# Kernel tuning notes

Measured on AMD Instinct MI355X. Metric: run time of the kernel, lower is better.

## Reference

```python
import jax, jax.numpy as jnp
import numpy as np

NEG = -9e15


def setup_inputs() -> dict:
    key = jax.random.key(0)
    k1, k2, k3, k4, k5 = jax.random.split(key, 5)
    N, D_IN, D_OUT = 8192, 512, 128
    x = jax.random.normal(k1, (N, D_IN), dtype=jnp.float32)
    adj = jax.random.randint(k2, (N, N), 0, 2, dtype=jnp.int32)
    W_fc = jax.random.normal(k3, (D_IN, D_OUT), dtype=jnp.float32) * (1.0 / np.sqrt(D_IN))
    w_a1 = jax.random.normal(k4, (D_OUT,), dtype=jnp.float32) * (1.0 / np.sqrt(D_OUT))
    w_a2 = jax.random.normal(k5, (D_OUT,), dtype=jnp.float32) * (1.0 / np.sqrt(D_OUT))
    return {"x": x, "adj": adj, "W_fc": W_fc, "w_a1": w_a1, "w_a2": w_a2}


def reference(x, adj, W_fc, w_a1, w_a2):
    # h = fc(x): [N, d_out]
    h = x @ W_fc
    # a1, a2: [N] projections; outer-sum scores a1[i] + a2[j] -> [N, N]
    a1 = h @ w_a1
    a2 = h @ w_a2
    scores = a1[:, None] + a2[None, :]
    # adjacency mask + row softmax
    scores = jnp.where(adj > 0, scores, jnp.float32(NEG))
    attention = jax.nn.softmax(scores, axis=-1)
    # weighted aggregation: [N, N] @ [N, d_out]
    out = attention @ h
    return out  # act == 'None', so no relu
```

## Files before the change

kernel.cpp:

```cpp
#include <hip/hip_runtime.h>
#include <hip/hip_bf16.h>


#define NN 8192
#define DIN 512
#define DOUT 128

typedef __attribute__((ext_vector_type(4))) int   int4v;
typedef __attribute__((ext_vector_type(4))) float f32x4;
typedef __attribute__((ext_vector_type(8))) short bf16x8;

static __device__ __forceinline__ unsigned short f2bf(float f) {
    unsigned u = __float_as_uint(f);
    return (unsigned short)((u + 0x7FFFu + ((u >> 16) & 1u)) >> 16);
}
static __device__ __forceinline__ float bf2f(unsigned short b) {
    return __uint_as_float((unsigned)b << 16);
}
static __device__ __forceinline__ void gload_lds16(const void* g, void* l) {
    __builtin_amdgcn_global_load_lds(
        (const __attribute__((address_space(1))) unsigned*)g,
        (__attribute__((address_space(3))) unsigned*)l, 16, 0, 0);
}
static __device__ __forceinline__ int4v ntld(const int* p) {
    return __builtin_nontemporal_load(reinterpret_cast<const int4v*>(p));
}
static __device__ __forceinline__ f32x4 ntldf4(const float* p) {
    return __builtin_nontemporal_load(reinterpret_cast<const f32x4*>(p));
}

__global__ __launch_bounds__(256) void k_cvtW(const float* __restrict__ W,
                                              unsigned short* __restrict__ WT) {
    __shared__ float s[8][128];
    const int t  = threadIdx.x;
    const int k0 = blockIdx.x * 8;
    {
        int idx = t * 4;
        int k = idx >> 7, d = idx & 127;
        float4 v = *reinterpret_cast<const float4*>(&W[(size_t)(k0 + k) * DOUT + d]);
        *reinterpret_cast<float4*>(&s[k][d]) = v;
    }
    __syncthreads();
    const int d  = t & 127;
    const int pl = t >> 7;
    unsigned short o[8];
    #pragma unroll
    for (int kk = 0; kk < 8; ++kk) {
        float f = s[kk][d];
        unsigned short hb = f2bf(f);
        o[kk] = pl ? f2bf(f - bf2f(hb)) : hb;
    }
    *reinterpret_cast<uint4*>(&WT[(size_t)pl * 128 * DIN + (size_t)d * DIN + k0]) =
        *reinterpret_cast<const uint4*>(o);
}

__global__ __launch_bounds__(256) void k_h(const float* __restrict__ x,
                                           const unsigned short* __restrict__ WT,
                                           const float* __restrict__ wa2,
                                           unsigned short* __restrict__ Gt) {
    __shared__ __align__(16) char xs[32768];
    __shared__ float red[4][16];
    __shared__ float es[16];
    const int t = threadIdx.x;
    const int w = t >> 6, l = t & 63;
    const int c = l & 15, g = l >> 4;
    const int j0 = blockIdx.x * 16;

    f32x4 xv[8];
    #pragma unroll
    for (int s = 0; s < 8; ++s) {
        int ii = t + s * 256;
        int r = ii >> 7, k4 = ii & 127;
        xv[s] = ntldf4(&x[(size_t)(j0 + r) * DIN + k4 * 4]);
    }
    #pragma unroll
    for (int s = 0; s < 8; ++s) {
        int ii = t + s * 256;
        int r = ii >> 7, k4 = ii & 127;
        unsigned byte0 = (unsigned)r * 1024 +
                         ((((unsigned)(k4 >> 1)) ^ ((unsigned)(r & 15))) << 4) + (k4 & 1) * 8;
        float vf[4] = {xv[s].x, xv[s].y, xv[s].z, xv[s].w};
        unsigned short hb[4], lb[4];
        #pragma unroll
        for (int e = 0; e < 4; ++e) { hb[e] = f2bf(vf[e]); lb[e] = f2bf(vf[e] - bf2f(hb[e])); }
        uint2 hv = {(unsigned)hb[0] | ((unsigned)hb[1] << 16),
                    (unsigned)hb[2] | ((unsigned)hb[3] << 16)};
        uint2 lv = {(unsigned)lb[0] | ((unsigned)lb[1] << 16),
                    (unsigned)lb[2] | ((unsigned)lb[3] << 16)};
        *reinterpret_cast<uint2*>(xs + byte0) = hv;
        *reinterpret_cast<uint2*>(xs + 16384 + byte0) = lv;
    }
    __syncthreads();

    const int wc0 = w * 32;
    const unsigned short* pB00 = WT + (size_t)(wc0 + c) * DIN + g * 8;
    const unsigned short* pB01 = pB00 + 16 * DIN;
    const unsigned short* pB10 = pB00 + 128 * DIN;
    const unsigned short* pB11 = pB01 + 128 * DIN;

    f32x4 acc0 = (f32x4)0.f, acc1 = (f32x4)0.f;
    const unsigned arow = (unsigned)c * 1024;
    const unsigned aswz = (unsigned)(c & 15);

    bf16x8 e00 = *reinterpret_cast<const bf16x8*>(pB00);
    bf16x8 e01 = *reinterpret_cast<const bf16x8*>(pB01);
    bf16x8 e10 = *reinterpret_cast<const bf16x8*>(pB10);
    bf16x8 e11 = *reinterpret_cast<const bf16x8*>(pB11);
    bf16x8 o00 = *reinterpret_cast<const bf16x8*>(pB00 + 32);
    bf16x8 o01 = *reinterpret_cast<const bf16x8*>(pB01 + 32);
    bf16x8 o10 = *reinterpret_cast<const bf16x8*>(pB10 + 32);
    bf16x8 o11 = *reinterpret_cast<const bf16x8*>(pB11 + 32);

    #pragma unroll
    for (int ks = 0; ks < 16; ks += 2) {
        {
            unsigned ab = arow + ((((unsigned)(ks * 4 + g)) ^ aswz) << 4);
            bf16x8 ahi = *reinterpret_cast<const bf16x8*>(xs + ab);
            bf16x8 alo = *reinterpret_cast<const bf16x8*>(xs + 16384 + ab);
            acc0 = __builtin_amdgcn_mfma_f32_16x16x32_bf16(ahi, e00, acc0, 0, 0, 0);
            acc1 = __builtin_amdgcn_mfma_f32_16x16x32_bf16(ahi, e01, acc1, 0, 0, 0);
            acc0 = __builtin_amdgcn_mfma_f32_16x16x32_bf16(ahi, e10, acc0, 0, 0, 0);
            acc1 = __builtin_amdgcn_mfma_f32_16x16x32_bf16(ahi, e11, acc1, 0, 0, 0);
            acc0 = __builtin_amdgcn_mfma_f32_16x16x32_bf16(alo, e00, acc0, 0, 0, 0);
            acc1 = __builtin_amdgcn_mfma_f32_16x16x32_bf16(alo, e01, acc1, 0, 0, 0);
            if (ks + 2 < 16) {
                e00 = *reinterpret_cast<const bf16x8*>(pB00 + (ks + 2) * 32);
                e01 = *reinterpret_cast<const bf16x8*>(pB01 + (ks + 2) * 32);
                e10 = *reinterpret_cast<const bf16x8*>(pB10 + (ks + 2) * 32);
                e11 = *reinterpret_cast<const bf16x8*>(pB11 + (ks + 2) * 32);
            }
        }
        {
            unsigned ab = arow + ((((unsigned)((ks + 1) * 4 + g)) ^ aswz) << 4);
            bf16x8 ahi = *reinterpret_cast<const bf16x8*>(xs + ab);
            bf16x8 alo = *reinterpret_cast<const bf16x8*>(xs + 16384 + ab);
            acc0 = __builtin_amdgcn_mfma_f32_16x16x32_bf16(ahi, o00, acc0, 0, 0, 0);
            acc1 = __builtin_amdgcn_mfma_f32_16x16x32_bf16(ahi, o01, acc1, 0, 0, 0);
            acc0 = __builtin_amdgcn_mfma_f32_16x16x32_bf16(ahi, o10, acc0, 0, 0, 0);
            acc1 = __builtin_amdgcn_mfma_f32_16x16x32_bf16(ahi, o11, acc1, 0, 0, 0);
            acc0 = __builtin_amdgcn_mfma_f32_16x16x32_bf16(alo, o00, acc0, 0, 0, 0);
            acc1 = __builtin_amdgcn_mfma_f32_16x16x32_bf16(alo, o01, acc1, 0, 0, 0);
            if (ks + 3 < 16) {
                o00 = *reinterpret_cast<const bf16x8*>(pB00 + (ks + 3) * 32);
                o01 = *reinterpret_cast<const bf16x8*>(pB01 + (ks + 3) * 32);
                o10 = *reinterpret_cast<const bf16x8*>(pB10 + (ks + 3) * 32);
                o11 = *reinterpret_cast<const bf16x8*>(pB11 + (ks + 3) * 32);
            }
        }
    }

    const float wl0 = wa2[wc0 + c];
    const float wl1 = wa2[wc0 + 16 + c];
    #pragma unroll
    for (int r = 0; r < 4; ++r) {
        float p = acc0[r] * wl0 + acc1[r] * wl1;
        p += __shfl_xor(p, 1); p += __shfl_xor(p, 2);
        p += __shfl_xor(p, 4); p += __shfl_xor(p, 8);
        if (c == 0) red[w][g * 4 + r] = p;
    }
    __syncthreads();
    if (t < 16) es[t] = expf(red[0][t] + red[1][t] + red[2][t] + red[3][t]);
    __syncthreads();

    {
        unsigned short b0[4], b1[4];
        #pragma unroll
        for (int r = 0; r < 4; ++r) {
            b0[r] = f2bf(acc0[r] * es[g * 4 + r]);
            b1[r] = f2bf(acc1[r] * es[g * 4 + r]);
        }
        uint2 v0 = {(unsigned)b0[0] | ((unsigned)b0[1] << 16),
                    (unsigned)b0[2] | ((unsigned)b0[3] << 16)};
        uint2 v1 = {(unsigned)b1[0] | ((unsigned)b1[1] << 16),
                    (unsigned)b1[2] | ((unsigned)b1[3] << 16)};
        *reinterpret_cast<uint2*>(&Gt[(size_t)(wc0 + c) * NN + j0 + g * 4]) = v0;
        *reinterpret_cast<uint2*>(&Gt[(size_t)(wc0 + 16 + c) * NN + j0 + g * 4]) = v1;
    }
    if (t < 8) {
        unsigned u = (unsigned)f2bf(es[t * 2]) | ((unsigned)f2bf(es[t * 2 + 1]) << 16);
        reinterpret_cast<unsigned*>(&Gt[(size_t)128 * NN + j0])[t] = u;
    }
}

__global__ __launch_bounds__(512) void k_gat(const int* __restrict__ adj,
                                             const unsigned short* __restrict__ Gt,
                                             float* __restrict__ out) {
    __shared__ __align__(16) char lds[127104];
    float* denp  = (float*)(lds + 122880);
    float* den_l = (float*)(lds + 126976);
    const int t = threadIdx.x;
    const int w = t >> 6, l = t & 63;
    const int c = l & 15, g = l >> 4;
    const int wm = w >> 2, wc = w & 3;
    const int row0 = blockIdx.x * 32;

    f32x4 acc0 = (f32x4)0.f, acc1 = (f32x4)0.f;
    float d0 = 0.f, d1 = 0.f;

    const int r0 = t >> 5;
    const int kg = t & 31;
    const int* ap0 = adj + (size_t)(row0 + r0) * NN + kg * 4;
    const int* ap1 = ap0 + (size_t)16 * NN;
    const unsigned short* ep = Gt + (size_t)128 * NN + kg * 4;
    const unsigned aw0 = (unsigned)r0 * 256 + (((unsigned)(kg * 8)) ^ (((unsigned)(r0 & 15)) << 4));
    const unsigned aw1 = aw0 + 4096;

    const unsigned abase = ((unsigned)(wm * 16 + c)) * 256;
    const unsigned afswz = ((unsigned)c) << 4;
    const unsigned br0 = (unsigned)(wc * 32 + c);
    const unsigned br1 = br0 + 16;
    const unsigned b0base = br0 * 256, b0swz = (br0 & 15) << 4;
    const unsigned b1base = br1 * 256, b1swz = (br1 & 15) << 4;

#define ISSUE_B(boff, ko) { char* Bn_ = lds + 24576 + (boff); \
    _Pragma("unroll") for (int s_ = 0; s_ < 4; ++s_) { \
        int ii_ = t + s_ * 512; int rb_ = ii_ >> 4, pb_ = ii_ & 15; \
        int gk_ = pb_ ^ (rb_ & 15); \
        gload_lds16(Gt + (size_t)rb_ * NN + (ko) + gk_ * 8, Bn_ + ii_ * 16); } }

#define LOAD_A(A0, A1, EV, ko) { A0 = ntld(ap0 + (ko)); A1 = ntld(ap1 + (ko)); \
    EV = *reinterpret_cast<const uint2*>(ep + (ko)); }

#define CONV_A(A0, A1, EV, aoff) { char* An_ = lds + (aoff); \
    unsigned u00_ = ((unsigned)A0.x | ((unsigned)A0.y << 16)) * 0x3F80u; \
    unsigned u01_ = ((unsigned)A0.z | ((unsigned)A0.w << 16)) * 0x3F80u; \
    unsigned u10_ = ((unsigned)A1.x | ((unsigned)A1.y << 16)) * 0x3F80u; \
    unsigned u11_ = ((unsigned)A1.z | ((unsigned)A1.w << 16)) * 0x3F80u; \
    uint2 w0_ = {u00_, u01_}, w1_ = {u10_, u11_}; \
    *reinterpret_cast<uint2*>(An_ + aw0) = w0_; \
    *reinterpret_cast<uint2*>(An_ + aw1) = w1_; \
    float e0_ = bf2f((unsigned short)(EV.x & 0xFFFFu)); \
    float e1_ = bf2f((unsigned short)(EV.x >> 16)); \
    float e2_ = bf2f((unsigned short)(EV.y & 0xFFFFu)); \
    float e3_ = bf2f((unsigned short)(EV.y >> 16)); \
    d0 += (A0.x ? e0_ : 0.f) + (A0.y ? e1_ : 0.f) + (A0.z ? e2_ : 0.f) + (A0.w ? e3_ : 0.f); \
    d1 += (A1.x ? e0_ : 0.f) + (A1.y ? e1_ : 0.f) + (A1.z ? e2_ : 0.f) + (A1.w ? e3_ : 0.f); }

#define COMPUTE(idx) { const char* Ab_ = lds + (idx) * 8192; \
    const char* Bb_ = lds + 24576 + (idx) * 32768; \
    _Pragma("unroll") for (int ks_ = 0; ks_ < 4; ++ks_) { \
        unsigned ko_ = (unsigned)(ks_ * 64 + g * 16); \
        bf16x8 av_ = *reinterpret_cast<const bf16x8*>(Ab_ + abase + (ko_ ^ afswz)); \
        bf16x8 b0_ = *reinterpret_cast<const bf16x8*>(Bb_ + b0base + (ko_ ^ b0swz)); \
        bf16x8 b1_ = *reinterpret_cast<const bf16x8*>(Bb_ + b1base + (ko_ ^ b1swz)); \
        acc0 = __builtin_amdgcn_mfma_f32_16x16x32_bf16(av_, b0_, acc0, 0, 0, 0); \
        acc1 = __builtin_amdgcn_mfma_f32_16x16x32_bf16(av_, b1_, acc1, 0, 0, 0); } }

#define SYNC7() { asm volatile("s_waitcnt vmcnt(7) lgkmcnt(0)" ::: "memory"); \
    __builtin_amdgcn_sched_barrier(0); __builtin_amdgcn_s_barrier(); \
    __builtin_amdgcn_sched_barrier(0); }
#define SYNC0() { asm volatile("s_waitcnt vmcnt(0) lgkmcnt(0)" ::: "memory"); \
    __builtin_amdgcn_sched_barrier(0); __builtin_amdgcn_s_barrier(); \
    __builtin_amdgcn_sched_barrier(0); }

    int4v eA0, eA1; uint2 eEv;
    int4v oA0, oA1; uint2 oEv;

    ISSUE_B(0, 0);
    LOAD_A(eA0, eA1, eEv, 0);
    ISSUE_B(32768, 128);
    LOAD_A(oA0, oA1, oEv, 128);
    CONV_A(eA0, eA1, eEv, 0);
    SYNC7();

    int i0 = 0, i1 = 1, i2 = 2;
    for (int kt = 0; kt < 62; kt += 2) {
        ISSUE_B(i2 * 32768, (kt + 2) * 128);
        LOAD_A(eA0, eA1, eEv, (kt + 2) * 128);
        COMPUTE(i0);
        CONV_A(oA0, oA1, oEv, i1 * 8192);
        SYNC7();
        { int tmp_ = i0; i0 = i1; i1 = i2; i2 = tmp_; }
        ISSUE_B(i2 * 32768, (kt + 3) * 128);
        LOAD_A(oA0, oA1, oEv, (kt + 3) * 128);
        COMPUTE(i0);
        CONV_A(eA0, eA1, eEv, i1 * 8192);
        SYNC7();
        { int tmp_ = i0; i0 = i1; i1 = i2; i2 = tmp_; }
    }
    COMPUTE(i0);
    CONV_A(oA0, oA1, oEv, i1 * 8192);
    SYNC0();
    { int tmp_ = i0; i0 = i1; i1 = i2; i2 = tmp_; }
    COMPUTE(i0);

#undef ISSUE_B
#undef LOAD_A
#undef CONV_A
#undef COMPUTE
#undef SYNC7
#undef SYNC0

    denp[r0 * 32 + kg] = d0;
    denp[(16 + r0) * 32 + kg] = d1;
    __syncthreads();
    if (t < 32) {
        float s = 0.f;
        #pragma unroll
        for (int q = 0; q < 32; ++q) s += denp[t * 32 + q];
        den_l[t] = s;
    }
    __syncthreads();

    #pragma unroll
    for (int r = 0; r < 4; ++r) {
        float inv = 1.0f / den_l[wm * 16 + g * 4 + r];
        float* orow = out + (size_t)(row0 + wm * 16 + g * 4 + r) * DOUT + wc * 32 + c;
        orow[0]  = acc0[r] * inv;
        orow[16] = acc1[r] * inv;
    }
}

extern "C" void kernel_launch(void* const* d_in, const int* in_sizes, int n_in,
                              void* d_out, int out_size, void* d_ws, size_t ws_size,
                              hipStream_t stream) {
    const float* x   = (const float*)d_in[0];
    const int*   adj = (const int*)d_in[1];
    const float* W   = (const float*)d_in[2];
    const float* wa2 = (const float*)d_in[4];
    float* out = (float*)d_out;

    char* ws = (char*)d_ws;
    unsigned short* WT = (unsigned short*)ws;
    unsigned short* Gt = (unsigned short*)(ws + 262144);

    k_cvtW<<< 64, 256, 0, stream>>>(W, WT);
    k_h   <<<512, 256, 0, stream>>>(x, WT, wa2, Gt);
    k_gat <<<256, 512, 0, stream>>>(adj, Gt, out);
}
```

Baseline: 410.3 us.

## Shrink GAT row tile to 16 rows and K-step to 64 for more blocks

Reworks the attention-aggregation kernel to process 16 rows per block with a 64-wide K step instead of 32 rows and 128. This doubles the grid to 512 blocks and cuts LDS use to about 72KB. The exp(a2) vector is preloaded once into LDS rather than re-fetched every K step. The goal is more resident blocks to hide latency on the adjacency stream, at the cost of reading Gt twice as often in total and running more sync iterations.

```diff
diff --git a/kernel.cpp b/kernel.cpp
--- a/kernel.cpp
+++ b/kernel.cpp
@@ -6,6 +6,7 @@
 #define DIN 512
 #define DOUT 128
 
+typedef __attribute__((ext_vector_type(2))) int   int2v;
 typedef __attribute__((ext_vector_type(4))) int   int4v;
 typedef __attribute__((ext_vector_type(4))) float f32x4;
 typedef __attribute__((ext_vector_type(8))) short bf16x8;
@@ -21,9 +22,6 @@
     __builtin_amdgcn_global_load_lds(
         (const __attribute__((address_space(1))) unsigned*)g,
         (__attribute__((address_space(3))) unsigned*)l, 16, 0, 0);
-}
-static __device__ __forceinline__ int4v ntld(const int* p) {
-    return __builtin_nontemporal_load(reinterpret_cast<const int4v*>(p));
 }
 static __device__ __forceinline__ f32x4 ntldf4(const float* p) {
     return __builtin_nontemporal_load(reinterpret_cast<const f32x4*>(p));
@@ -182,104 +180,97 @@
     }
 }
 
-__global__ __launch_bounds__(512) void k_gat(const int* __restrict__ adj,
-                                             const unsigned short* __restrict__ Gt,
-                                             float* __restrict__ out) {
-    __shared__ __align__(16) char lds[127104];
-    float* denp  = (float*)(lds + 122880);
-    float* den_l = (float*)(lds + 126976);
+__global__ __launch_bounds__(512, 4) void k_gat(const int* __restrict__ adj,
+                                                const unsigned short* __restrict__ Gt,
+                                                float* __restrict__ out) {
+    __shared__ __align__(16) char lds[73792];
+    float* denp  = (float*)(lds + 71680);
+    float* den_l = (float*)(lds + 73728);
     const int t = threadIdx.x;
     const int w = t >> 6, l = t & 63;
     const int c = l & 15, g = l >> 4;
-    const int wm = w >> 2, wc = w & 3;
-    const int row0 = blockIdx.x * 32;
-
-    f32x4 acc0 = (f32x4)0.f, acc1 = (f32x4)0.f;
-    float d0 = 0.f, d1 = 0.f;
-
-    const int r0 = t >> 5;
-    const int kg = t & 31;
-    const int* ap0 = adj + (size_t)(row0 + r0) * NN + kg * 4;
-    const int* ap1 = ap0 + (size_t)16 * NN;
-    const unsigned short* ep = Gt + (size_t)128 * NN + kg * 4;
-    const unsigned aw0 = (unsigned)r0 * 256 + (((unsigned)(kg * 8)) ^ (((unsigned)(r0 & 15)) << 4));
-    const unsigned aw1 = aw0 + 4096;
-
-    const unsigned abase = ((unsigned)(wm * 16 + c)) * 256;
-    const unsigned afswz = ((unsigned)c) << 4;
-    const unsigned br0 = (unsigned)(wc * 32 + c);
-    const unsigned br1 = br0 + 16;
-    const unsigned b0base = br0 * 256, b0swz = (br0 & 15) << 4;
-    const unsigned b1base = br1 * 256, b1swz = (br1 & 15) << 4;
-
-#define ISSUE_B(boff, ko) { char* Bn_ = lds + 24576 + (boff); \
-    _Pragma("unroll") for (int s_ = 0; s_ < 4; ++s_) { \
-        int ii_ = t + s_ * 512; int rb_ = ii_ >> 4, pb_ = ii_ & 15; \
-        int gk_ = pb_ ^ (rb_ & 15); \
-        gload_lds16(Gt + (size_t)rb_ * NN + (ko) + gk_ * 8, Bn_ + ii_ * 16); } }
-
-#define LOAD_A(A0, A1, EV, ko) { A0 = ntld(ap0 + (ko)); A1 = ntld(ap1 + (ko)); \
-    EV = *reinterpret_cast<const uint2*>(ep + (ko)); }
-
-#define CONV_A(A0, A1, EV, aoff) { char* An_ = lds + (aoff); \
-    unsigned u00_ = ((unsigned)A0.x | ((unsigned)A0.y << 16)) * 0x3F80u; \
-    unsigned u01_ = ((unsigned)A0.z | ((unsigned)A0.w << 16)) * 0x3F80u; \
-    unsigned u10_ = ((unsigned)A1.x | ((unsigned)A1.y << 16)) * 0x3F80u; \
-    unsigned u11_ = ((unsigned)A1.z | ((unsigned)A1.w << 16)) * 0x3F80u; \
-    uint2 w0_ = {u00_, u01_}, w1_ = {u10_, u11_}; \
-    *reinterpret_cast<uint2*>(An_ + aw0) = w0_; \
-    *reinterpret_cast<uint2*>(An_ + aw1) = w1_; \
-    float e0_ = bf2f((unsigned short)(EV.x & 0xFFFFu)); \
-    float e1_ = bf2f((unsigned short)(EV.x >> 16)); \
-    float e2_ = bf2f((unsigned short)(EV.y & 0xFFFFu)); \
-    float e3_ = bf2f((unsigned short)(EV.y >> 16)); \
-    d0 += (A0.x ? e0_ : 0.f) + (A0.y ? e1_ : 0.f) + (A0.z ? e2_ : 0.f) + (A0.w ? e3_ : 0.f); \
-    d1 += (A1.x ? e0_ : 0.f) + (A1.y ? e1_ : 0.f) + (A1.z ? e2_ : 0.f) + (A1.w ? e3_ : 0.f); }
-
-#define COMPUTE(idx) { const char* Ab_ = lds + (idx) * 8192; \
-    const char* Bb_ = lds + 24576 + (idx) * 32768; \
-    _Pragma("unroll") for (int ks_ = 0; ks_ < 4; ++ks_) { \
+    const int row0 = blockIdx.x * 16;
+
+    f32x4 acc = (f32x4)0.f;
+    float dden = 0.f;
+
+    const int ar  = t >> 5;
+    const int kg2 = t & 31;
+    const int* ap = adj + (size_t)(row0 + ar) * NN + kg2 * 2;
+    const unsigned awb = (unsigned)ar * 128 +
+                         (((unsigned)(kg2 * 4)) ^ (((unsigned)(ar & 7)) << 4));
+
+    const int brow0 = t >> 3,          bpb0 = t & 7;
+    const int brow1 = (t + 512) >> 3,  bpb1 = (t + 512) & 7;
+    const unsigned short* bsrc0 = Gt + (size_t)brow0 * NN + (bpb0 ^ (brow0 & 7)) * 8;
+    const unsigned short* bsrc1 = Gt + (size_t)brow1 * NN + (bpb1 ^ (brow1 & 7)) * 8;
+    const unsigned bd0 = (unsigned)t * 16, bd1 = bd0 + 8192;
+
+    const unsigned abase = (unsigned)c * 128, aswz = ((unsigned)(c & 7)) << 4;
+    const unsigned brf = (unsigned)(w * 16 + c);
+    const unsigned bbase = brf * 128, bswz = ((unsigned)(brf & 7)) << 4;
+
+#define ISSUE_B(bi, ko) { char* Bn_ = lds + 16384 + (bi) * 16384; \
+    gload_lds16(bsrc0 + (ko), Bn_ + bd0); \
+    gload_lds16(bsrc1 + (ko), Bn_ + bd1); }
+
+#define LOAD_A(A, ko) { A = *reinterpret_cast<const int2v*>(ap + (ko)); }
+
+#define CONV_A(A, bi, ko) { char* An_ = lds + 65536 + (bi) * 2048; \
+    unsigned u_ = (((unsigned)A.x) | (((unsigned)A.y) << 16)) * 0x3F80u; \
+    *reinterpret_cast<unsigned*>(An_ + awb) = u_; \
+    unsigned eu_ = *reinterpret_cast<const unsigned*>(lds + ((ko) + kg2 * 2) * 2); \
+    float e0_ = bf2f((unsigned short)(eu_ & 0xFFFFu)); \
+    float e1_ = bf2f((unsigned short)(eu_ >> 16)); \
+    dden += (A.x ? e0_ : 0.f) + (A.y ? e1_ : 0.f); }
+
+#define COMPUTE(bi) { const char* Ab_ = lds + 65536 + (bi) * 2048; \
+    const char* Bb_ = lds + 16384 + (bi) * 16384; \
+    _Pragma("unroll") for (int ks_ = 0; ks_ < 2; ++ks_) { \
         unsigned ko_ = (unsigned)(ks_ * 64 + g * 16); \
-        bf16x8 av_ = *reinterpret_cast<const bf16x8*>(Ab_ + abase + (ko_ ^ afswz)); \
-        bf16x8 b0_ = *reinterpret_cast<const bf16x8*>(Bb_ + b0base + (ko_ ^ b0swz)); \
-        bf16x8 b1_ = *reinterpret_cast<const bf16x8*>(Bb_ + b1base + (ko_ ^ b1swz)); \
-        acc0 = __builtin_amdgcn_mfma_f32_16x16x32_bf16(av_, b0_, acc0, 0, 0, 0); \
-        acc1 = __builtin_amdgcn_mfma_f32_16x16x32_bf16(av_, b1_, acc1, 0, 0, 0); } }
-
-#define SYNC7() { asm volatile("s_waitcnt vmcnt(7) lgkmcnt(0)" ::: "memory"); \
+        bf16x8 av_ = *reinterpret_cast<const bf16x8*>(Ab_ + abase + (ko_ ^ aswz)); \
+        bf16x8 bv_ = *reinterpret_cast<const bf16x8*>(Bb_ + bbase + (ko_ ^ bswz)); \
+        acc = __builtin_amdgcn_mfma_f32_16x16x32_bf16(av_, bv_, acc, 0, 0, 0); } }
+
+#define SYNC3() { asm volatile("s_waitcnt vmcnt(3) lgkmcnt(0)" ::: "memory"); \
     __builtin_amdgcn_sched_barrier(0); __builtin_amdgcn_s_barrier(); \
     __builtin_amdgcn_sched_barrier(0); }
 #define SYNC0() { asm volatile("s_waitcnt vmcnt(0) lgkmcnt(0)" ::: "memory"); \
     __builtin_amdgcn_sched_barrier(0); __builtin_amdgcn_s_barrier(); \
     __builtin_amdgcn_sched_barrier(0); }
 
-    int4v eA0, eA1; uint2 eEv;
-    int4v oA0, oA1; uint2 oEv;
-
-    ISSUE_B(0, 0);
-    LOAD_A(eA0, eA1, eEv, 0);
-    ISSUE_B(32768, 128);
-    LOAD_A(oA0, oA1, oEv, 128);
-    CONV_A(eA0, eA1, eEv, 0);
-    SYNC7();
+    int2v eA, oA;
+
+    {
+        const unsigned short* esrc = Gt + (size_t)128 * NN;
+        gload_lds16(esrc + t * 8,          lds + t * 16);
+        gload_lds16(esrc + (t + 512) * 8,  lds + 8192 + t * 16);
+    }
+    ISSUE_B(0, 0);   LOAD_A(eA, 0);
+    ISSUE_B(1, 64);  LOAD_A(oA, 64);
+    asm volatile("s_waitcnt vmcnt(3)" ::: "memory");
+    __builtin_amdgcn_sched_barrier(0);
+    __builtin_amdgcn_s_barrier();
+    CONV_A(eA, 0, 0);
+    asm volatile("s_waitcnt lgkmcnt(0)" ::: "memory");
+    __builtin_amdgcn_sched_barrier(0);
+    __builtin_amdgcn_s_barrier();
 
     int i0 = 0, i1 = 1, i2 = 2;
-    for (int kt = 0; kt < 62; kt += 2) {
-        ISSUE_B(i2 * 32768, (kt + 2) * 128);
-        LOAD_A(eA0, eA1, eEv, (kt + 2) * 128);
+    for (int kt = 0; kt < 126; kt += 2) {
+        ISSUE_B(i2, (kt + 2) * 64);  LOAD_A(eA, (kt + 2) * 64);
         COMPUTE(i0);
-        CONV_A(oA0, oA1, oEv, i1 * 8192);
-        SYNC7();
+        CONV_A(oA, i1, (kt + 1) * 64);
+        SYNC3();
         { int tmp_ = i0; i0 = i1; i1 = i2; i2 = tmp_; }
-        ISSUE_B(i2 * 32768, (kt + 3) * 128);
-        LOAD_A(oA0, oA1, oEv, (kt + 3) * 128);
+        ISSUE_B(i2, (kt + 3) * 64);  LOAD_A(oA, (kt + 3) * 64);
         COMPUTE(i0);
-        CONV_A(eA0, eA1, eEv, i1 * 8192);
-        SYNC7();
+        CONV_A(eA, i1, (kt + 2) * 64);
+        SYNC3();
         { int tmp_ = i0; i0 = i1; i1 = i2; i2 = tmp_; }
     }
     COMPUTE(i0);
-    CONV_A(oA0, oA1, oEv, i1 * 8192);
+    CONV_A(oA, i1, 127 * 64);
     SYNC0();
     { int tmp_ = i0; i0 = i1; i1 = i2; i2 = tmp_; }
     COMPUTE(i0);
@@ -288,13 +279,12 @@
 #undef LOAD_A
 #undef CONV_A
 #undef COMPUTE
-#undef SYNC7
+#undef SYNC3
 #undef SYNC0
 
-    denp[r0 * 32 + kg] = d0;
-    denp[(16 + r0) * 32 + kg] = d1;
-    __syncthreads();
-    if (t < 32) {
+    denp[ar * 32 + kg2] = dden;
+    __syncthreads();
+    if (t < 16) {
         float s = 0.f;
         #pragma unroll
         for (int q = 0; q < 32; ++q) s += denp[t * 32 + q];
@@ -304,10 +294,8 @@
 
     #pragma unroll
     for (int r = 0; r < 4; ++r) {
-        float inv = 1.0f / den_l[wm * 16 + g * 4 + r];
-        float* orow = out + (size_t)(row0 + wm * 16 + g * 4 + r) * DOUT + wc * 32 + c;
-        orow[0]  = acc0[r] * inv;
-        orow[16] = acc1[r] * inv;
+        float inv = 1.0f / den_l[g * 4 + r];
+        out[(size_t)(row0 + g * 4 + r) * DOUT + w * 16 + c] = acc[r] * inv;
     }
 }
 
@@ -326,5 +314,5 @@
 
     k_cvtW<<< 64, 256, 0, stream>>>(W, WT);
     k_h   <<<512, 256, 0, stream>>>(x, WT, wa2, Gt);
-    k_gat <<<256, 512, 0, stream>>>(adj, Gt, out);
-}
+    k_gat <<<512, 512, 0, stream>>>(adj, Gt, out);
+}
```

Measured after the change: 428.7 us. +4.5%, slower.
